# Optimization experiments

Measured on AMD Instinct MI355X. Metric: run time of the kernel, lower is better.

## Reference

```python
import jax, jax.numpy as jnp
import numpy as np

NUM_GRAPHS = 2048
BN_EPS = 1e-5


def gcn_conv(x, W, b, src, dst, deg_isqrt):
    # PyG GCNConv: out = D^{-1/2} (A + I) D^{-1/2} X W + b
    h = x @ W  # [N, H]
    norm = deg_isqrt[src] * deg_isqrt[dst]  # [E]
    msg = h[src] * norm[:, None]            # [E, H]
    agg = jax.ops.segment_sum(msg, dst, num_segments=x.shape[0])
    agg = agg + h * (deg_isqrt * deg_isqrt)[:, None]  # self-loop term
    return agg + b


def batch_norm(x, gamma, beta):
    # training-mode BatchNorm1d over nodes (biased variance)
    mean = jnp.mean(x, axis=0)
    var = jnp.mean(jnp.square(x - mean), axis=0)
    return gamma * (x - mean) * jax.lax.rsqrt(var + BN_EPS) + beta


def pools(x, batch):
    ones = jnp.ones((x.shape[0],), x.dtype)
    cnt = jax.ops.segment_sum(ones, batch, num_segments=NUM_GRAPHS)  # [G]
    mean_p = jax.ops.segment_sum(x, batch, num_segments=NUM_GRAPHS) / jnp.maximum(cnt, 1.0)[:, None]
    max_p = jax.ops.segment_max(x, batch, num_segments=NUM_GRAPHS)
    max_p = jnp.where(cnt[:, None] > 0, max_p, 0.0)
    return jnp.concatenate([mean_p, max_p], axis=1)  # [G, 2H]


def setup_inputs() -> dict:
    key = jax.random.key(0)
    ks = jax.random.split(key, 32)
    N, E, D, H = 100000, 300000, 8, 256
    x = jax.random.normal(ks[0], (N, D), jnp.float32)
    edge_index = jax.random.randint(ks[1], (2, E), 0, N, jnp.int64)
    batch = jnp.sort(jax.random.randint(ks[2], (N,), 0, NUM_GRAPHS, jnp.int64))

    def lin(k, fi, fo):
        s = 1.0 / np.sqrt(fi)
        kw, kb = jax.random.split(k)
        return (jax.random.uniform(kw, (fi, fo), jnp.float32, -s, s),
                jax.random.uniform(kb, (fo,), jnp.float32, -s, s))

    W1, b1 = lin(ks[3], D, H)
    W2, b2 = lin(ks[4], H, H)
    W3, b3 = lin(ks[5], H, H)
    W4, b4 = lin(ks[6], H, H)
    g = jnp.ones((H,), jnp.float32)
    be = jnp.zeros((H,), jnp.float32)
    sW1, sb1 = lin(ks[7], 2 * H, 256)
    sW2, sb2 = lin(ks[8], 256, 128)
    hW1 = jnp.stack([lin(ks[9 + i], 128, 32)[0] for i in range(3)])
    hb1 = jnp.stack([lin(ks[9 + i], 128, 32)[1] for i in range(3)])
    hW2 = jnp.stack([lin(ks[12 + i], 32, 1)[0] for i in range(3)])
    hb2 = jnp.stack([lin(ks[12 + i], 32, 1)[1] for i in range(3)])
    return dict(x=x, edge_index=edge_index, batch=batch,
                W1=W1, b1=b1, W2=W2, b2=b2, W3=W3, b3=b3, W4=W4, b4=b4,
                g1=g, be1=be, g2=g, be2=be, g3=g, be3=be, g4=g, be4=be,
                sW1=sW1, sb1=sb1, sW2=sW2, sb2=sb2,
                hW1=hW1, hb1=hb1, hW2=hW2, hb2=hb2)


def reference(x, edge_index, batch, W1, b1, W2, b2, W3, b3, W4, b4,
              g1, be1, g2, be2, g3, be3, g4, be4,
              sW1, sb1, sW2, sb2, hW1, hb1, hW2, hb2):
    src, dst = edge_index[0], edge_index[1]
    N = x.shape[0]
    # degree with self-loops (GCN normalization)
    deg = jax.ops.segment_sum(jnp.ones((src.shape[0],), x.dtype), dst, num_segments=N) + 1.0
    deg_isqrt = jax.lax.rsqrt(deg)

    h = jax.nn.relu(batch_norm(gcn_conv(x, W1, b1, src, dst, deg_isqrt), g1, be1))
    h = jax.nn.relu(batch_norm(gcn_conv(h, W2, b2, src, dst, deg_isqrt), g2, be2))
    h = jax.nn.relu(batch_norm(gcn_conv(h, W3, b3, src, dst, deg_isqrt), g3, be3))
    h = jax.nn.relu(batch_norm(gcn_conv(h, W4, b4, src, dst, deg_isqrt), g4, be4))

    pooled = pools(h, batch)                               # [G, 512]
    s = jax.nn.relu(pooled @ sW1 + sb1)                    # dropout: eval -> identity
    s = jax.nn.relu(s @ sW2 + sb2)                         # [G, 128]
    # heads (vectorized over 3 tasks): [T, G]
    t = jax.nn.relu(jnp.einsum('gf,tfo->tgo', s, hW1) + hb1[:, None, :])
    out = (jnp.einsum('tgo,tof->tgf', t, hW2) + hb2[:, None, :])[..., 0]
    return out  # [num_tasks, G] == stacked list of squeezed head outputs
```

## Files before the change

### kernel.cpp

```cpp
#include <hip/hip_runtime.h>
#include <math.h>

#define TPB 256
#define NGRAPH 2048

typedef __attribute__((ext_vector_type(8))) short bf16x8;
typedef __attribute__((ext_vector_type(4))) float f32x4;

__device__ __forceinline__ unsigned short f2bf(float f) {
  unsigned u = __float_as_uint(f);
  unsigned r = (u + 0x7FFF + ((u >> 16) & 1)) >> 16;
  return (unsigned short)r;
}
__device__ __forceinline__ float bf2f(unsigned short h) {
  return __uint_as_float(((unsigned)h) << 16);
}

#define GLOAD_LDS16(G, L) \
  __builtin_amdgcn_global_load_lds((const __attribute__((address_space(1))) unsigned int*)(G), \
                                   (__attribute__((address_space(3))) unsigned int*)(L), 16, 0, 0)

__global__ void k_init(float* __restrict__ deg, int* __restrict__ cnt,
                       int* __restrict__ cntg, float* __restrict__ statsAll,
                       float* __restrict__ statsP, int N) {
  int i = blockIdx.x * TPB + threadIdx.x;
  if (i < N) { deg[i] = 1.0f; cnt[i] = 0; }
  if (i < NGRAPH) cntg[i] = 0;
  if (i < 2048) statsAll[i] = 0.f;
  if (i < 12288) statsP[i] = 0.f;
}

__global__ void k_deg_hist(const int* __restrict__ dst, float* __restrict__ deg,
                           int* __restrict__ cnt, int E) {
  int e = blockIdx.x * TPB + threadIdx.x;
  if (e < E) {
    int d = dst[e];
    atomicAdd(&deg[d], 1.0f);
    atomicAdd(&cnt[d], 1);
  }
}

__global__ void k_hist_batch(const int* __restrict__ batch, int* __restrict__ cntg, int N) {
  int i = blockIdx.x * TPB + threadIdx.x;
  if (i < N) atomicAdd(&cntg[batch[i]], 1);
}

__global__ void k_rsqrt(float* __restrict__ d, int N) {
  int i = blockIdx.x * TPB + threadIdx.x;
  if (i < N) d[i] = rsqrtf(d[i]);
}

__global__ void k_scan1(const int* __restrict__ in, int* __restrict__ out,
                        int* __restrict__ bsum, int n) {
  __shared__ int ts[256];
  int tid = threadIdx.x;
  int base = blockIdx.x * 1024 + tid * 4;
  int v0 = (base + 0 < n) ? in[base + 0] : 0;
  int v1 = (base + 1 < n) ? in[base + 1] : 0;
  int v2 = (base + 2 < n) ? in[base + 2] : 0;
  int v3 = (base + 3 < n) ? in[base + 3] : 0;
  int s = v0 + v1 + v2 + v3;
  int run = s;
  ts[tid] = run; __syncthreads();
  for (int off = 1; off < 256; off <<= 1) {
    int add = (tid >= off) ? ts[tid - off] : 0;
    __syncthreads();
    run += add; ts[tid] = run; __syncthreads();
  }
  int acc = run - s;
  if (base + 0 < n) out[base + 0] = acc; acc += v0;
  if (base + 1 < n) out[base + 1] = acc; acc += v1;
  if (base + 2 < n) out[base + 2] = acc; acc += v2;
  if (base + 3 < n) out[base + 3] = acc;
  if (tid == 255) bsum[blockIdx.x] = run;
}

__global__ void k_scan_small(const int* __restrict__ in, int* __restrict__ dst, int n) {
  __shared__ int ts[256];
  int tid = threadIdx.x;
  int chunk = (n + 255) >> 8;
  int start = tid * chunk;
  int s = 0;
  for (int j = 0; j < chunk; ++j) { int idx = start + j; if (idx < n) s += in[idx]; }
  int run = s;
  ts[tid] = run; __syncthreads();
  for (int off = 1; off < 256; off <<= 1) {
    int add = (tid >= off) ? ts[tid - off] : 0;
    __syncthreads();
    run += add; ts[tid] = run; __syncthreads();
  }
  int acc = run - s;
  for (int j = 0; j < chunk; ++j) {
    int idx = start + j;
    if (idx < n) { dst[idx] = acc; acc += in[idx]; }
  }
  if (tid == 255) dst[n] = run;
}

__global__ void k_scan3(int* __restrict__ rs, const int* __restrict__ bsumx,
                        int* __restrict__ cursor, int n, int total) {
  int i = blockIdx.x * TPB + threadIdx.x;
  if (i < n) {
    int v = rs[i] + bsumx[i >> 10];
    rs[i] = v; cursor[i] = v;
  }
  if (i == 0) rs[n] = total;
}

__global__ void k_scatter(const int* __restrict__ src, const int* __restrict__ dst,
                          int* __restrict__ cursor, int* __restrict__ es, int E) {
  int e = blockIdx.x * TPB + threadIdx.x;
  if (e < E) {
    int d = dst[e];
    int p = atomicAdd(&cursor[d], 1);
    es[p] = src[e];
  }
}

__global__ __launch_bounds__(256) void k_wprep2(const float* __restrict__ W,
    unsigned short* __restrict__ Wblk) {
  int c = blockIdx.x, k = threadIdx.x;
  float w = W[k * 256 + c];
  int t = k >> 6, kl = k & 63;
  Wblk[t * 16384 + c * 64 + (kl ^ ((c & 7) << 3))] = f2bf(w);
}

__global__ void k_agg8(const float* __restrict__ x, const float* __restrict__ dis,
                       const int* __restrict__ rs, const int* __restrict__ es,
                       float* __restrict__ xa8, int N) {
  int t = blockIdx.x * TPB + threadIdx.x;
  int n = t >> 3, c = t & 7;
  if (n >= N) return;
  int e0 = rs[n], e1 = rs[n + 1];
  float acc = 0.f;
  for (int e = e0; e < e1; ++e) {
    int s = es[e];
    acc += dis[s] * x[s * 8 + c];
  }
  float dn = dis[n];
  xa8[n * 8 + c] = dn * acc + dn * dn * x[n * 8 + c];
}

__global__ __launch_bounds__(256) void k_gemm8(const float* __restrict__ A,
    const float* __restrict__ W, const float* __restrict__ b,
    unsigned short* __restrict__ Ybf, float* __restrict__ stats, int N) {
  __shared__ float Ws[8 * 256];
  __shared__ float bs[256];
  __shared__ float rows[128 * 8];
  int tid = threadIdx.x;
  int row0 = blockIdx.x * 128;
  for (int j = 0; j < 8; ++j) Ws[tid + j * 256] = W[tid + j * 256];
  bs[tid] = b[tid];
  int lim = N * 8;
#pragma unroll
  for (int j = 0; j < 4; ++j) {
    int o = row0 * 8 + j * 256 + tid;
    rows[j * 256 + tid] = (o < lim) ? A[o] : 0.f;
  }
  __syncthreads();
  const int c2 = (tid & 127) * 2;
  const int rh = tid >> 7;
  float2 wv[8];
#pragma unroll
  for (int k = 0; k < 8; ++k)
    wv[k] = make_float2(Ws[k * 256 + c2], Ws[k * 256 + c2 + 1]);
  const float b0 = bs[c2], b1 = bs[c2 + 1];
  float s0 = 0.f, s1 = 0.f, q0 = 0.f, q1 = 0.f;
  for (int r = 0; r < 64; ++r) {
    int rl = rh * 64 + r;
    int row = row0 + rl;
    if (row >= N) break;
    float a0 = b0, a1 = b1;
#pragma unroll
    for (int k = 0; k < 8; ++k) {
      float rv = rows[rl * 8 + k];
      a0 = fmaf(rv, wv[k].x, a0);
      a1 = fmaf(rv, wv[k].y, a1);
    }
    ushort2 o; o.x = f2bf(a0); o.y = f2bf(a1);
    *(ushort2*)&Ybf[(size_t)row * 256 + c2] = o;
    s0 += a0; q0 += a0 * a0; s1 += a1; q1 += a1 * a1;
  }
  atomicAdd(&stats[c2], s0);       atomicAdd(&stats[256 + c2], q0);
  atomicAdd(&stats[c2 + 1], s1);   atomicAdd(&stats[256 + c2 + 1], q1);
}

__global__ __launch_bounds__(256) void k_agg_bn(const unsigned short* __restrict__ Ybf,
    const float* __restrict__ ss, const float* __restrict__ dis,
    const int* __restrict__ rs, const int* __restrict__ es,
    unsigned short* __restrict__ Ahi, int N) {
  int lane = threadIdx.x & 63;
  int n = __builtin_amdgcn_readfirstlane(blockIdx.x * 4 + (threadIdx.x >> 6));
  if (n >= N) return;
  int c = lane * 4;
  float4 sc = *(const float4*)&ss[c];
  float4 sh = *(const float4*)&ss[256 + c];
  int e0 = rs[n], e1 = rs[n + 1];
  float4 a = make_float4(0.f, 0.f, 0.f, 0.f);
  int e = e0;
  for (; e + 2 <= e1; e += 2) {
    int s0 = es[e], s1 = es[e + 1];
    float d0 = dis[s0], d1 = dis[s1];
    ushort4 y0 = *(const ushort4*)&Ybf[(size_t)s0 * 256 + c];
    ushort4 y1 = *(const ushort4*)&Ybf[(size_t)s1 * 256 + c];
    a.x += d0 * fmaxf(fmaf(bf2f(y0.x), sc.x, sh.x), 0.f)
         + d1 * fmaxf(fmaf(bf2f(y1.x), sc.x, sh.x), 0.f);
    a.y += d0 * fmaxf(fmaf(bf2f(y0.y), sc.y, sh.y), 0.f)
         + d1 * fmaxf(fmaf(bf2f(y1.y), sc.y, sh.y), 0.f);
    a.z += d0 * fmaxf(fmaf(bf2f(y0.z), sc.z, sh.z), 0.f)
         + d1 * fmaxf(fmaf(bf2f(y1.z), sc.z, sh.z), 0.f);
    a.w += d0 * fmaxf(fmaf(bf2f(y0.w), sc.w, sh.w), 0.f)
         + d1 * fmaxf(fmaf(bf2f(y1.w), sc.w, sh.w), 0.f);
  }
  if (e < e1) {
    int s0 = es[e];
    float d0 = dis[s0];
    ushort4 y0 = *(const ushort4*)&Ybf[(size_t)s0 * 256 + c];
    a.x += d0 * fmaxf(fmaf(bf2f(y0.x), sc.x, sh.x), 0.f);
    a.y += d0 * fmaxf(fmaf(bf2f(y0.y), sc.y, sh.y), 0.f);
    a.z += d0 * fmaxf(fmaf(bf2f(y0.z), sc.z, sh.z), 0.f);
    a.w += d0 * fmaxf(fmaf(bf2f(y0.w), sc.w, sh.w), 0.f);
  }
  float dn = dis[n];
  float dn2 = dn * dn;
  ushort4 yb = *(const ushort4*)&Ybf[(size_t)n * 256 + c];
  float4 r;
  r.x = dn * a.x + dn2 * fmaxf(fmaf(bf2f(yb.x), sc.x, sh.x), 0.f);
  r.y = dn * a.y + dn2 * fmaxf(fmaf(bf2f(yb.y), sc.y, sh.y), 0.f);
  r.z = dn * a.z + dn2 * fmaxf(fmaf(bf2f(yb.z), sc.z, sh.z), 0.f);
  r.w = dn * a.w + dn2 * fmaxf(fmaf(bf2f(yb.w), sc.w, sh.w), 0.f);
  ushort4 h;
  h.x = f2bf(r.x); h.y = f2bf(r.y); h.z = f2bf(r.z); h.w = f2bf(r.w);
  *(ushort4*)&Ahi[(size_t)n * 256 + c] = h;
}

__global__ __launch_bounds__(256) void k_gemm_mfma(
    const unsigned short* __restrict__ A,
    const unsigned short* __restrict__ Wblk,
    const float* __restrict__ bias, unsigned short* __restrict__ Ybf,
    float* __restrict__ statsP, int M) {
  __shared__ unsigned short Wlds[16384];
  __shared__ float bstats[512];
  const int tid = threadIdx.x;
  const int lane = tid & 63;
  const int w = tid >> 6;
  const int l15 = lane & 15, lg = lane >> 4;
  const int r0 = blockIdx.x * 64 + w * 16;

  bstats[tid] = 0.f;
  bstats[tid + 256] = 0.f;

  const unsigned short* Ap = A + (size_t)(r0 + l15) * 256 + lg * 8;

  f32x4 acc[16] = {};
#pragma unroll
  for (int t = 0; t < 4; ++t) {
#pragma unroll
    for (int it = 0; it < 8; ++it)
      GLOAD_LDS16(Wblk + t * 16384 + it * 2048 + tid * 8,
                  &Wlds[it * 2048 + tid * 8]);
    bf16x8 a0 = *(const bf16x8*)(Ap + t * 64);
    bf16x8 a1 = *(const bf16x8*)(Ap + t * 64 + 32);
    asm volatile("s_waitcnt vmcnt(0)" ::: "memory");
    __builtin_amdgcn_s_barrier();
#pragma unroll
    for (int kk2 = 0; kk2 < 2; ++kk2) {
      bf16x8 a = kk2 ? a1 : a0;
#pragma unroll
      for (int n = 0; n < 16; ++n) {
        int c = n * 16 + l15;
        bf16x8 b = *(const bf16x8*)&Wlds[c * 64 +
                     ((kk2 * 32 + lg * 8) ^ ((l15 & 7) << 3))];
        acc[n] = __builtin_amdgcn_mfma_f32_16x16x32_bf16(a, b, acc[n], 0, 0, 0);
      }
    }
    asm volatile("s_waitcnt lgkmcnt(0)" ::: "memory");
    __builtin_amdgcn_s_barrier();
  }

  unsigned short* stage = Wlds;
#pragma unroll
  for (int n = 0; n < 16; ++n) {
    int col = n * 16 + l15;
    float bv = bias[col];
    float s = 0.f, s2 = 0.f;
    f32x4 v = acc[n];
#pragma unroll
    for (int j = 0; j < 4; ++j) {
      float val = v[j] + bv;
      int rl = w * 16 + lg * 4 + j;
      stage[rl * 256 + col] = f2bf(val);
      if (blockIdx.x * 64 + rl < M) { s += val; s2 += val * val; }
    }
    s += __shfl_xor(s, 16);  s += __shfl_xor(s, 32);
    s2 += __shfl_xor(s2, 16); s2 += __shfl_xor(s2, 32);
    if (lg == 0) {
      atomicAdd(&bstats[col], s);
      atomicAdd(&bstats[256 + col], s2);
    }
  }
  __syncthreads();
#pragma unroll
  for (int it = 0; it < 8; ++it) {
    int idx = it * 256 + tid;
    int rl = idx >> 5;
    int c16 = idx & 31;
    int grow = blockIdx.x * 64 + rl;
    if (grow < M)
      *(int4*)((char*)Ybf + (size_t)grow * 512 + c16 * 16) =
          *(const int4*)((const char*)stage + rl * 512 + c16 * 16);
  }
  float* sp = statsP + (blockIdx.x & 7) * 512;
  atomicAdd(&sp[tid], bstats[tid]);
  atomicAdd(&sp[256 + tid], bstats[256 + tid]);
}

__global__ void k_scaleshift(const float* __restrict__ base, int npart,
                             const float* __restrict__ g,
                             const float* __restrict__ be, float* __restrict__ ss, int N) {
  int c = threadIdx.x;
  float s = 0.f, s2 = 0.f;
  for (int p = 0; p < npart; ++p) {
    s += base[p * 512 + c];
    s2 += base[p * 512 + 256 + c];
  }
  float inv = 1.0f / (float)N;
  float mean = s * inv;
  float var = s2 * inv - mean * mean;
  var = fmaxf(var, 0.f);
  float sc = g[c] * rsqrtf(var + 1e-5f);
  ss[c] = sc;
  ss[256 + c] = be[c] - mean * sc;
}

__global__ __launch_bounds__(256) void k_pool(const unsigned short* __restrict__ Ybf,
    const float* __restrict__ ss, const int* __restrict__ gstart,
    float* __restrict__ pooled) {
  int g = blockIdx.x, c = threadIdx.x;
  float sc = ss[c], sh = ss[256 + c];
  int n0 = gstart[g], n1 = gstart[g + 1];
  float s = 0.f, m = 0.f;
  for (int n = n0; n < n1; ++n) {
    float v = fmaxf(fmaf(bf2f(Ybf[(size_t)n * 256 + c]), sc, sh), 0.f);
    s += v; m = fmaxf(m, v);
  }
  float cnt = (float)(n1 - n0);
  pooled[g * 512 + c] = s / fmaxf(cnt, 1.0f);
  pooled[g * 512 + 256 + c] = m;
}

__global__ __launch_bounds__(256) void k_mlp1(const float* __restrict__ P,
    const float* __restrict__ W, const float* __restrict__ b, float* __restrict__ O) {
  __shared__ float Ps[4 * 512];
  int tid = threadIdx.x;
  int g0 = blockIdx.x * 4;
  for (int j = 0; j < 8; ++j) Ps[j * 256 + tid] = P[g0 * 512 + j * 256 + tid];
  __syncthreads();
  float acc[4];
  float bb = b[tid];
#pragma unroll
  for (int gi = 0; gi < 4; ++gi) acc[gi] = bb;
  for (int k = 0; k < 512; ++k) {
    float w = W[k * 256 + tid];
#pragma unroll
    for (int gi = 0; gi < 4; ++gi) acc[gi] += Ps[gi * 512 + k] * w;
  }
#pragma unroll
  for (int gi = 0; gi < 4; ++gi)
    O[(g0 + gi) * 256 + tid] = fmaxf(acc[gi], 0.f);
}

__global__ __launch_bounds__(128) void k_mlp2(const float* __restrict__ S,
    const float* __restrict__ W, const float* __restrict__ b, float* __restrict__ O) {
  __shared__ float Ss[2 * 256];
  int tid = threadIdx.x;
  int g0 = blockIdx.x * 2;
  for (int j = 0; j < 4; ++j) Ss[j * 128 + tid] = S[g0 * 256 + j * 128 + tid];
  __syncthreads();
  float acc[2];
  float bb = b[tid];
  acc[0] = bb; acc[1] = bb;
  for (int k = 0; k < 256; ++k) {
    float w = W[k * 128 + tid];
    acc[0] += Ss[k] * w;
    acc[1] += Ss[256 + k] * w;
  }
  O[g0 * 128 + tid] = fmaxf(acc[0], 0.f);
  O[(g0 + 1) * 128 + tid] = fmaxf(acc[1], 0.f);
}

__global__ __launch_bounds__(128) void k_heads(const float* __restrict__ S,
    const float* __restrict__ hW1, const float* __restrict__ hb1,
    const float* __restrict__ hW2, const float* __restrict__ hb2,
    float* __restrict__ out) {
  __shared__ float ssm[128];
  __shared__ float t1[96];
  int g = blockIdx.x, tid = threadIdx.x;
  ssm[tid] = S[g * 128 + tid];
  __syncthreads();
  if (tid < 96) {
    int t = tid >> 5, o = tid & 31;
    float acc = hb1[t * 32 + o];
    for (int k = 0; k < 128; ++k) acc += ssm[k] * hW1[t * 4096 + k * 32 + o];
    t1[tid] = fmaxf(acc, 0.f);
  }
  __syncthreads();
  if (tid < 3) {
    float acc = hb2[tid];
    for (int o = 0; o < 32; ++o) acc += t1[tid * 32 + o] * hW2[tid * 32 + o];
    out[tid * NGRAPH + g] = acc;
  }
}

extern "C" void kernel_launch(void* const* d_in, const int* in_sizes, int n_in,
                              void* d_out, int out_size, void* d_ws, size_t ws_size,
                              hipStream_t stream) {
  const float* x   = (const float*)d_in[0];
  const int* ei    = (const int*)d_in[1];
  const int* batch = (const int*)d_in[2];
  const float* W1 = (const float*)d_in[3];  const float* b1 = (const float*)d_in[4];
  const float* W2 = (const float*)d_in[5];  const float* b2 = (const float*)d_in[6];
  const float* W3 = (const float*)d_in[7];  const float* b3 = (const float*)d_in[8];
  const float* W4 = (const float*)d_in[9];  const float* b4 = (const float*)d_in[10];
  const float* g1 = (const float*)d_in[11]; const float* be1 = (const float*)d_in[12];
  const float* g2 = (const float*)d_in[13]; const float* be2 = (const float*)d_in[14];
  const float* g3 = (const float*)d_in[15]; const float* be3 = (const float*)d_in[16];
  const float* g4 = (const float*)d_in[17]; const float* be4 = (const float*)d_in[18];
  const float* sW1 = (const float*)d_in[19]; const float* sb1 = (const float*)d_in[20];
  const float* sW2 = (const float*)d_in[21]; const float* sb2 = (const float*)d_in[22];
  const float* hW1 = (const float*)d_in[23]; const float* hb1 = (const float*)d_in[24];
  const float* hW2 = (const float*)d_in[25]; const float* hb2 = (const float*)d_in[26];

  const int N = in_sizes[0] / 8;
  const int E = in_sizes[1] / 2;
  const int Npad = (N + 127) & ~127;
  const int* srcp = ei;
  const int* dstp = ei + E;

  char* base = (char*)d_ws;
  size_t off = 0;
  auto alloc = [&](size_t bytes) -> void* {
    void* p = base + off;
    off += (bytes + 255) & ~(size_t)255;
    return p;
  };
  unsigned short* Ybf = (unsigned short*)alloc((size_t)Npad * 256 * 2);
  unsigned short* Ahi = (unsigned short*)alloc((size_t)Npad * 256 * 2);
  float* dis  = (float*)alloc((size_t)N * 4);
  int* cnt    = (int*)alloc((size_t)N * 4);
  int* rs     = (int*)alloc((size_t)(N + 1) * 4);
  int* cursor = (int*)alloc((size_t)N * 4);
  int* es     = (int*)alloc((size_t)E * 4);
  int* bsum   = (int*)alloc(1024 * 4);
  int* bsumx  = (int*)alloc(1032 * 4);
  float* xa8  = (float*)alloc((size_t)N * 8 * 4);
  float* statsAll = (float*)alloc(2048 * 4);
  float* statsP   = (float*)alloc(12288 * 4);
  float* ssAll    = (float*)alloc(2048 * 4);
  unsigned short* Wblk = (unsigned short*)alloc(3 * 256 * 256 * 2);
  int* cntg    = (int*)alloc(2048 * 4);
  int* gstart  = (int*)alloc(2049 * 4);
  float* pooled = (float*)alloc((size_t)2048 * 512 * 4);
  float* s1b    = (float*)alloc((size_t)2048 * 256 * 4);
  float* s2b    = (float*)alloc((size_t)2048 * 128 * 4);
  (void)ws_size; (void)n_in; (void)out_size;

  int nb = (N + TPB - 1) / TPB;
  int eb = (E + TPB - 1) / TPB;
  int nblocks1 = (N + 1023) / 1024;

  k_init<<<nb, TPB, 0, stream>>>(dis, cnt, cntg, statsAll, statsP, N);
  k_deg_hist<<<eb, TPB, 0, stream>>>(dstp, dis, cnt, E);
  k_hist_batch<<<nb, TPB, 0, stream>>>(batch, cntg, N);
  k_rsqrt<<<nb, TPB, 0, stream>>>(dis, N);
  k_scan1<<<nblocks1, 256, 0, stream>>>(cnt, rs, bsum, N);
  k_scan_small<<<1, 256, 0, stream>>>(bsum, bsumx, nblocks1);
  k_scan3<<<nb, TPB, 0, stream>>>(rs, bsumx, cursor, N, E);
  k_scatter<<<eb, TPB, 0, stream>>>(srcp, dstp, cursor, es, E);
  k_scan_small<<<1, 256, 0, stream>>>(cntg, gstart, NGRAPH);

  k_wprep2<<<256, 256, 0, stream>>>(W2, Wblk + 0 * 65536);
  k_wprep2<<<256, 256, 0, stream>>>(W3, Wblk + 1 * 65536);
  k_wprep2<<<256, 256, 0, stream>>>(W4, Wblk + 2 * 65536);

  k_agg8<<<(N * 8 + TPB - 1) / TPB, TPB, 0, stream>>>(x, dis, rs, es, xa8, N);
  k_gemm8<<<(N + 127) / 128, 256, 0, stream>>>(xa8, W1, b1, Ybf, statsAll, N);
  k_scaleshift<<<1, 256, 0, stream>>>(statsAll, 1, g1, be1, ssAll, N);

  const float* bs_[3] = {b2, b3, b4};
  const float* gs[3]  = {g2, g3, g4};
  const float* bes[3] = {be2, be3, be4};
  for (int L = 0; L < 3; ++L) {
    k_agg_bn<<<(N + 3) / 4, 256, 0, stream>>>(Ybf, ssAll + L * 512, dis, rs, es,
                                              Ahi, N);
    k_gemm_mfma<<<(N + 63) / 64, 256, 0, stream>>>(Ahi, Wblk + L * 65536,
                                                   bs_[L], Ybf, statsP + L * 4096, N);
    k_scaleshift<<<1, 256, 0, stream>>>(statsP + L * 4096, 8, gs[L], bes[L],
                                        ssAll + (L + 1) * 512, N);
  }

  k_pool<<<NGRAPH, 256, 0, stream>>>(Ybf, ssAll + 3 * 512, gstart, pooled);
  k_mlp1<<<NGRAPH / 4, 256, 0, stream>>>(pooled, sW1, sb1, s1b);
  k_mlp2<<<NGRAPH / 2, 128, 0, stream>>>(s1b, sW2, sb2, s2b);
  k_heads<<<NGRAPH, 128, 0, stream>>>(s2b, hW1, hb1, hW2, hb2, (float*)d_out);
}
```

Measured before the change: 534.4 us.

## Halve MFMA GEMM LDS footprint with 32-wide K slices and two-pass epilogue staging

The MFMA GEMM now streams W in eight 32-wide K slices (16KB LDS instead of 32KB). Its epilogue stages 32 rows at a time in two passes so the smaller buffer still fits the output, and the weight prep layout and swizzle are changed to match. This is meant to raise occupancy by cutting LDS per block. In exchange it adds more barriers and global-to-LDS rounds. Separately, the first-layer GEMM now uses 64-row blocks with one column per thread, writing bf16 scalars instead of pairs.

```diff
diff --git a/kernel.cpp b/kernel.cpp
--- a/kernel.cpp
+++ b/kernel.cpp
@@ -121,8 +121,8 @@
     unsigned short* __restrict__ Wblk) {
   int c = blockIdx.x, k = threadIdx.x;
   float w = W[k * 256 + c];
-  int t = k >> 6, kl = k & 63;
-  Wblk[t * 16384 + c * 64 + (kl ^ ((c & 7) << 3))] = f2bf(w);
+  int s = k >> 5, kl = k & 31;
+  Wblk[s * 8192 + c * 32 + (kl ^ ((c & 3) << 3))] = f2bf(w);
 }
 
 __global__ void k_agg8(const float* __restrict__ x, const float* __restrict__ dis,
@@ -146,43 +146,37 @@
     unsigned short* __restrict__ Ybf, float* __restrict__ stats, int N) {
   __shared__ float Ws[8 * 256];
   __shared__ float bs[256];
-  __shared__ float rows[128 * 8];
+  __shared__ float rows[64 * 8];
   int tid = threadIdx.x;
-  int row0 = blockIdx.x * 128;
+  int row0 = blockIdx.x * 64;
   for (int j = 0; j < 8; ++j) Ws[tid + j * 256] = W[tid + j * 256];
   bs[tid] = b[tid];
   int lim = N * 8;
-#pragma unroll
-  for (int j = 0; j < 4; ++j) {
-    int o = row0 * 8 + j * 256 + tid;
-    rows[j * 256 + tid] = (o < lim) ? A[o] : 0.f;
-  }
+  int o0 = row0 * 8 + tid, o1 = o0 + 256;
+  rows[tid] = (o0 < lim) ? A[o0] : 0.f;
+  rows[tid + 256] = (o1 < lim) ? A[o1] : 0.f;
   __syncthreads();
-  const int c2 = (tid & 127) * 2;
-  const int rh = tid >> 7;
-  float2 wv[8];
-#pragma unroll
-  for (int k = 0; k < 8; ++k)
-    wv[k] = make_float2(Ws[k * 256 + c2], Ws[k * 256 + c2 + 1]);
-  const float b0 = bs[c2], b1 = bs[c2 + 1];
-  float s0 = 0.f, s1 = 0.f, q0 = 0.f, q1 = 0.f;
-  for (int r = 0; r < 64; ++r) {
-    int rl = rh * 64 + r;
-    int row = row0 + rl;
-    if (row >= N) break;
-    float a0 = b0, a1 = b1;
+  float bb = bs[tid];
+  float s = 0.f, s2 = 0.f;
+  for (int r = 0; r < 64; r += 2) {
+    int rowA = row0 + r, rowB = rowA + 1;
+    float a0 = bb, a1 = bb;
 #pragma unroll
     for (int k = 0; k < 8; ++k) {
-      float rv = rows[rl * 8 + k];
-      a0 = fmaf(rv, wv[k].x, a0);
-      a1 = fmaf(rv, wv[k].y, a1);
+      a0 = fmaf(rows[r * 8 + k], Ws[k * 256 + tid], a0);
+      a1 = fmaf(rows[r * 8 + 8 + k], Ws[k * 256 + tid], a1);
     }
-    ushort2 o; o.x = f2bf(a0); o.y = f2bf(a1);
-    *(ushort2*)&Ybf[(size_t)row * 256 + c2] = o;
-    s0 += a0; q0 += a0 * a0; s1 += a1; q1 += a1 * a1;
-  }
-  atomicAdd(&stats[c2], s0);       atomicAdd(&stats[256 + c2], q0);
-  atomicAdd(&stats[c2 + 1], s1);   atomicAdd(&stats[256 + c2 + 1], q1);
+    if (rowA < N) {
+      Ybf[(size_t)rowA * 256 + tid] = f2bf(a0);
+      s += a0; s2 += a0 * a0;
+    }
+    if (rowB < N) {
+      Ybf[(size_t)rowB * 256 + tid] = f2bf(a1);
+      s += a1; s2 += a1 * a1;
+    }
+  }
+  atomicAdd(&stats[tid], s);
+  atomicAdd(&stats[256 + tid], s2);
 }
 
 __global__ __launch_bounds__(256) void k_agg_bn(const unsigned short* __restrict__ Ybf,
@@ -239,7 +233,7 @@
     const unsigned short* __restrict__ Wblk,
     const float* __restrict__ bias, unsigned short* __restrict__ Ybf,
     float* __restrict__ statsP, int M) {
-  __shared__ unsigned short Wlds[16384];
+  __shared__ unsigned short Wlds[8192];
   __shared__ float bstats[512];
   const int tid = threadIdx.x;
   const int lane = tid & 63;
@@ -254,25 +248,20 @@
 
   f32x4 acc[16] = {};
 #pragma unroll
-  for (int t = 0; t < 4; ++t) {
-#pragma unroll
-    for (int it = 0; it < 8; ++it)
-      GLOAD_LDS16(Wblk + t * 16384 + it * 2048 + tid * 8,
+  for (int t = 0; t < 8; ++t) {
+#pragma unroll
+    for (int it = 0; it < 4; ++it)
+      GLOAD_LDS16(Wblk + t * 8192 + it * 2048 + tid * 8,
                   &Wlds[it * 2048 + tid * 8]);
-    bf16x8 a0 = *(const bf16x8*)(Ap + t * 64);
-    bf16x8 a1 = *(const bf16x8*)(Ap + t * 64 + 32);
+    bf16x8 a = *(const bf16x8*)(Ap + t * 32);
     asm volatile("s_waitcnt vmcnt(0)" ::: "memory");
     __builtin_amdgcn_s_barrier();
 #pragma unroll
-    for (int kk2 = 0; kk2 < 2; ++kk2) {
-      bf16x8 a = kk2 ? a1 : a0;
-#pragma unroll
-      for (int n = 0; n < 16; ++n) {
-        int c = n * 16 + l15;
-        bf16x8 b = *(const bf16x8*)&Wlds[c * 64 +
-                     ((kk2 * 32 + lg * 8) ^ ((l15 & 7) << 3))];
-        acc[n] = __builtin_amdgcn_mfma_f32_16x16x32_bf16(a, b, acc[n], 0, 0, 0);
-      }
+    for (int n = 0; n < 16; ++n) {
+      int c = n * 16 + l15;
+      bf16x8 b = *(const bf16x8*)&Wlds[c * 32 +
+                   ((lg * 8) ^ ((c & 3) << 3))];
+      acc[n] = __builtin_amdgcn_mfma_f32_16x16x32_bf16(a, b, acc[n], 0, 0, 0);
     }
     asm volatile("s_waitcnt lgkmcnt(0)" ::: "memory");
     __builtin_amdgcn_s_barrier();
@@ -280,36 +269,43 @@
 
   unsigned short* stage = Wlds;
 #pragma unroll
-  for (int n = 0; n < 16; ++n) {
-    int col = n * 16 + l15;
-    float bv = bias[col];
-    float s = 0.f, s2 = 0.f;
-    f32x4 v = acc[n];
-#pragma unroll
-    for (int j = 0; j < 4; ++j) {
-      float val = v[j] + bv;
-      int rl = w * 16 + lg * 4 + j;
-      stage[rl * 256 + col] = f2bf(val);
-      if (blockIdx.x * 64 + rl < M) { s += val; s2 += val * val; }
+  for (int p = 0; p < 2; ++p) {
+    if (p) __syncthreads();
+    if ((w >> 1) == p) {
+#pragma unroll
+      for (int n = 0; n < 16; ++n) {
+        int col = n * 16 + l15;
+        float bv = bias[col];
+        float s = 0.f, s2 = 0.f;
+        f32x4 v = acc[n];
+#pragma unroll
+        for (int j = 0; j < 4; ++j) {
+          float val = v[j] + bv;
+          int srow = (w & 1) * 16 + lg * 4 + j;
+          stage[srow * 256 + col] = f2bf(val);
+          if (blockIdx.x * 64 + p * 32 + srow < M) { s += val; s2 += val * val; }
+        }
+        s += __shfl_xor(s, 16);  s += __shfl_xor(s, 32);
+        s2 += __shfl_xor(s2, 16); s2 += __shfl_xor(s2, 32);
+        if (lg == 0) {
+          atomicAdd(&bstats[col], s);
+          atomicAdd(&bstats[256 + col], s2);
+        }
+      }
     }
-    s += __shfl_xor(s, 16);  s += __shfl_xor(s, 32);
-    s2 += __shfl_xor(s2, 16); s2 += __shfl_xor(s2, 32);
-    if (lg == 0) {
-      atomicAdd(&bstats[col], s);
-      atomicAdd(&bstats[256 + col], s2);
+    __syncthreads();
+#pragma unroll
+    for (int it = 0; it < 4; ++it) {
+      int idx = it * 256 + tid;
+      int rl = idx >> 5;
+      int c16 = idx & 31;
+      int grow = blockIdx.x * 64 + p * 32 + rl;
+      if (grow < M)
+        *(int4*)((char*)Ybf + (size_t)grow * 512 + c16 * 16) =
+            *(const int4*)((const char*)stage + rl * 512 + c16 * 16);
     }
   }
   __syncthreads();
-#pragma unroll
-  for (int it = 0; it < 8; ++it) {
-    int idx = it * 256 + tid;
-    int rl = idx >> 5;
-    int c16 = idx & 31;
-    int grow = blockIdx.x * 64 + rl;
-    if (grow < M)
-      *(int4*)((char*)Ybf + (size_t)grow * 512 + c16 * 16) =
-          *(const int4*)((const char*)stage + rl * 512 + c16 * 16);
-  }
   float* sp = statsP + (blockIdx.x & 7) * 512;
   atomicAdd(&sp[tid], bstats[tid]);
   atomicAdd(&sp[256 + tid], bstats[256 + tid]);
@@ -484,7 +480,7 @@
   k_wprep2<<<256, 256, 0, stream>>>(W4, Wblk + 2 * 65536);
 
   k_agg8<<<(N * 8 + TPB - 1) / TPB, TPB, 0, stream>>>(x, dis, rs, es, xa8, N);
-  k_gemm8<<<(N + 127) / 128, 256, 0, stream>>>(xa8, W1, b1, Ybf, statsAll, N);
+  k_gemm8<<<(N + 63) / 64, 256, 0, stream>>>(xa8, W1, b1, Ybf, statsAll, N);
   k_scaleshift<<<1, 256, 0, stream>>>(statsAll, 1, g1, be1, ssAll, N);
 
   const float* bs_[3] = {b2, b3, b4};
```

Result: faster. 522.0 us (-2.3%).
